# Kernel tuning notes

Measured on AMD Instinct MI355X. Metric: run time of the kernel, lower is better.

## Reference

```python
import jax, jax.numpy as jnp
import numpy as np


def _mlp(x, w1, b1, w2, b2):
    # generic 2-layer MLP (stand-in for ConfiguredModule's combine_mlp / embedding_mlp)
    return jax.nn.gelu(x @ w1 + b1) @ w2 + b2


def setup_inputs() -> dict:
    key = jax.random.key(0)
    ks = jax.random.split(key, 8)
    B, N, A = 8, 128, 64          # molecules, atoms, nfeature
    Rr, Ra = 32, 16               # radial / angular geometry shifts
    P = N * (N - 1) // 2          # 8128 atom pairs
    d_pair, H, nembed = 32, 512, 256

    def rnd(k, shp, scale=1.0):
        return jax.random.normal(k, shp, dtype=jnp.float32) * scale

    return {
        "gr": rnd(ks[0], (B, N, Rr, N), 0.1),
        "ga": rnd(ks[1], (B, N, Ra, P), 0.1),
        "afv": rnd(ks[2], (B, N, A)),
        # combine_mlp: 2A -> 2A -> d_pair
        "cw1": rnd(ks[3], (2 * A, 2 * A), 1.0 / np.sqrt(2 * A)),
        "cb1": jnp.zeros((2 * A,), jnp.float32),
        "cw2": rnd(ks[4], (2 * A, d_pair), 1.0 / np.sqrt(2 * A)),
        "cb2": jnp.zeros((d_pair,), jnp.float32),
        # embedding_mlp: Rr*A + Ra*d_pair -> H -> nembed
        "ew1": rnd(ks[5], (Rr * A + Ra * d_pair, H), 1.0 / np.sqrt(Rr * A + Ra * d_pair)),
        "eb1": jnp.zeros((H,), jnp.float32),
        "ew2": rnd(ks[6], (H, nembed), 1.0 / np.sqrt(H)),
        "eb2": jnp.zeros((nembed,), jnp.float32),
    }


def reference(gr, ga, afv, cw1, cb1, cw2, cb2, ew1, eb1, ew2, eb2):
    B, N, A = afv.shape
    # _combine_afv_1: pairwise outer sum/product, upper-triangular (i<j) pairs.
    # Instead of materializing [B, 2A, N, N] and masking, gather pairs directly
    # (row-major i<j order matches torch's triu boolean-mask indexing).
    ii, jj = jnp.triu_indices(N, k=1)           # [P]
    ai = afv[:, ii, :]                           # [B, P, A]
    aj = afv[:, jj, :]                           # [B, P, A]
    afv_pair = jnp.concatenate([ai + aj, ai * aj], axis=-1)  # [B, P, 2A]
    afv_pair = _mlp(afv_pair, cw1, cb1, cw2, cb2)            # [B, P, d_pair]

    # grv = matmul(gr, afv[:, None]) : [B, N, Rr, N] @ [B, 1, N, A] -> [B, N, Rr, A]
    grv = jnp.einsum('bnrm,bma->bnra', gr, afv).reshape(B, N, -1)
    # gav = matmul(ga, afv_pair[:, None]) : [B, N, Ra, P] @ [B, 1, P, d] -> [B, N, Ra, d]
    gav = jnp.einsum('bnap,bpd->bnad', ga, afv_pair).reshape(B, N, -1)

    aef = _mlp(jnp.concatenate([grv, gav], axis=-1), ew1, eb1, ew2, eb2)  # [B, N, nembed]
    return aef, afv
```

## Files before the change

### kernel.cpp

```cpp
#include <hip/hip_runtime.h>
#include <math.h>

#define BB 8
#define NN 128
#define AA 64
#define RR 32
#define RA 16
#define PP 8128
#define DP 32
#define HH 512
#define EE 256
#define XDIM 2560

static constexpr size_t WS_PAIRT = 0;
static constexpr size_t WS_XB    = WS_PAIRT + (size_t)BB*DP*PP/2;
static constexpr size_t WS_EW1B  = WS_XB + (size_t)BB*NN*XDIM/2;
static constexpr size_t WS_CW1T  = WS_EW1B + (size_t)HH*XDIM/2;
static constexpr size_t WS_CW2T  = WS_CW1T + (size_t)128*128/2;
static constexpr size_t WS_EW2B  = WS_CW2T + (size_t)DP*128/2;
static constexpr size_t WS_HB    = WS_EW2B + (size_t)EE*HH/2;

typedef __attribute__((ext_vector_type(8))) short bf16x8;
typedef __attribute__((ext_vector_type(4))) float f32x4;

__device__ __forceinline__ float gelu_f(float x) {
    float u = 0.7978845608028654f * (x + 0.044715f * x * x * x);
    float au = fabsf(u);
    float e = __expf(-2.0f * au);
    float th = (1.0f - e) / (1.0f + e);
    th = copysignf(th, u);
    return 0.5f * x * (1.0f + th);
}

__device__ __forceinline__ unsigned short f2bf(float x) {
    union { float f; unsigned u; } v; v.f = x;
    unsigned r = v.u + 0x7fffu + ((v.u >> 16) & 1u);
    return (unsigned short)(r >> 16);
}

__device__ __forceinline__ bf16x8 pack_bf16x8(float4 a, float4 b) {
    bf16x8 r;
    r[0] = (short)f2bf(a.x); r[1] = (short)f2bf(a.y);
    r[2] = (short)f2bf(a.z); r[3] = (short)f2bf(a.w);
    r[4] = (short)f2bf(b.x); r[5] = (short)f2bf(b.y);
    r[6] = (short)f2bf(b.z); r[7] = (short)f2bf(b.w);
    return r;
}

__global__ __launch_bounds__(256) void prep_k(
    const float* __restrict__ cw1, const float* __restrict__ cw2,
    unsigned short* __restrict__ cw1T, unsigned short* __restrict__ cw2T)
{
    const int bid = blockIdx.x, t = threadIdx.x;
    if (bid < 16) {
        int idx = bid * 256 + t;
        int n = idx >> 5;
        int k0 = (idx & 31) * 4;
        ushort4 o;
        o.x = f2bf(cw1[(size_t)(k0 + 0) * 128 + n]);
        o.y = f2bf(cw1[(size_t)(k0 + 1) * 128 + n]);
        o.z = f2bf(cw1[(size_t)(k0 + 2) * 128 + n]);
        o.w = f2bf(cw1[(size_t)(k0 + 3) * 128 + n]);
        *(ushort4*)(cw1T + (size_t)n * 128 + k0) = o;
    } else {
        int idx = (bid - 16) * 256 + t;
        int d = idx >> 5;
        int k0 = (idx & 31) * 4;
        ushort4 o;
        o.x = f2bf(cw2[(size_t)(k0 + 0) * DP + d]);
        o.y = f2bf(cw2[(size_t)(k0 + 1) * DP + d]);
        o.z = f2bf(cw2[(size_t)(k0 + 2) * DP + d]);
        o.w = f2bf(cw2[(size_t)(k0 + 3) * DP + d]);
        *(ushort4*)(cw2T + (size_t)d * 128 + k0) = o;
    }
}

__global__ __launch_bounds__(256) void stage1_k(
    const float* __restrict__ afv, const unsigned short* __restrict__ cw1T,
    const float* __restrict__ cb1, const unsigned short* __restrict__ cw2T,
    const float* __restrict__ cb2, unsigned short* __restrict__ pairT)
{
    __shared__ unsigned short sm[16384];
    __shared__ int iis[64], jjs[64];
    const int bid = blockIdx.x;
    const int t = threadIdx.x;
    const int w = t >> 6, lane = t & 63;
    const int lm = lane & 15, lg = lane >> 4;

    const int b = bid / 127;
    const int pbase = (bid % 127) * 64;
    unsigned short* X = sm;
    unsigned short* Hs = sm + 8192;

    if (t < 64) {
        int p = pbase + t;
        int i = 0;
        while (i < 126) {
            int nx = i + 1;
            int off = nx * 127 - (nx * (nx - 1)) / 2;
            if (off <= p) i = nx; else break;
        }
        int off = i * 127 - (i * (i - 1)) / 2;
        iis[t] = i;
        jjs[t] = i + 1 + (p - off);
    }
    __syncthreads();
    {
        int pp = t & 63, seg = t >> 6;
        const float* ar = afv + (size_t)(b * NN + iis[pp]) * AA + seg * 16;
        const float* br = afv + (size_t)(b * NN + jjs[pp]) * AA + seg * 16;
        float4 xa = *(const float4*)(ar),     xb2 = *(const float4*)(ar + 4);
        float4 xc = *(const float4*)(ar + 8), xd = *(const float4*)(ar + 12);
        float4 ya = *(const float4*)(br),     yb = *(const float4*)(br + 4);
        float4 yc = *(const float4*)(br + 8), yd = *(const float4*)(br + 12);
        float4 s0 = make_float4(xa.x + ya.x, xa.y + ya.y, xa.z + ya.z, xa.w + ya.w);
        float4 s1 = make_float4(xb2.x + yb.x, xb2.y + yb.y, xb2.z + yb.z, xb2.w + yb.w);
        float4 s2 = make_float4(xc.x + yc.x, xc.y + yc.y, xc.z + yc.z, xc.w + yc.w);
        float4 s3 = make_float4(xd.x + yd.x, xd.y + yd.y, xd.z + yd.z, xd.w + yd.w);
        float4 p0 = make_float4(xa.x * ya.x, xa.y * ya.y, xa.z * ya.z, xa.w * ya.w);
        float4 p1 = make_float4(xb2.x * yb.x, xb2.y * yb.y, xb2.z * yb.z, xb2.w * yb.w);
        float4 p2 = make_float4(xc.x * yc.x, xc.y * yc.y, xc.z * yc.z, xc.w * yc.w);
        float4 p3 = make_float4(xd.x * yd.x, xd.y * yd.y, xd.z * yd.z, xd.w * yd.w);
        int gs = seg * 2, gp = 8 + seg * 2, sw = pp & 7;
        *(bf16x8*)(X + pp * 128 + (((gs + 0) ^ sw) * 8)) = pack_bf16x8(s0, s1);
        *(bf16x8*)(X + pp * 128 + (((gs + 1) ^ sw) * 8)) = pack_bf16x8(s2, s3);
        *(bf16x8*)(X + pp * 128 + (((gp + 0) ^ sw) * 8)) = pack_bf16x8(p0, p1);
        *(bf16x8*)(X + pp * 128 + (((gp + 1) ^ sw) * 8)) = pack_bf16x8(p2, p3);
    }
    __syncthreads();
    const int wn = w * 32;
    f32x4 acc1[4][2];
    #pragma unroll
    for (int i = 0; i < 4; ++i)
        #pragma unroll
        for (int j = 0; j < 2; ++j) acc1[i][j] = 0.f;
    #pragma unroll
    for (int ks = 0; ks < 4; ++ks) {
        int g = ks * 4 + lg;
        bf16x8 a[4];
        #pragma unroll
        for (int mi = 0; mi < 4; ++mi) {
            int row = mi * 16 + lm;
            a[mi] = *(const bf16x8*)(X + row * 128 + ((g ^ (row & 7)) * 8));
        }
        #pragma unroll
        for (int ni = 0; ni < 2; ++ni) {
            bf16x8 bv = *(const bf16x8*)(cw1T + (size_t)(wn + ni * 16 + lm) * 128 +
                                         ks * 32 + lg * 8);
            #pragma unroll
            for (int mi = 0; mi < 4; ++mi)
                acc1[mi][ni] = __builtin_amdgcn_mfma_f32_16x16x32_bf16(
                    a[mi], bv, acc1[mi][ni], 0, 0, 0);
        }
    }
    #pragma unroll
    for (int ni = 0; ni < 2; ++ni) {
        int n = wn + ni * 16 + lm;
        float bb = cb1[n];
        int gn = n >> 3, ne = n & 7;
        #pragma unroll
        for (int mi = 0; mi < 4; ++mi)
            #pragma unroll
            for (int r = 0; r < 4; ++r) {
                int row = mi * 16 + lg * 4 + r;
                Hs[row * 128 + ((gn ^ (row & 7)) * 8 + ne)] =
                    f2bf(gelu_f(acc1[mi][ni][r] + bb));
            }
    }
    __syncthreads();
    f32x4 acc2[2];
    acc2[0] = 0.f; acc2[1] = 0.f;
    #pragma unroll
    for (int ks = 0; ks < 4; ++ks) {
        int row = w * 16 + lm;
        int g = ks * 4 + lg;
        bf16x8 a2 = *(const bf16x8*)(Hs + row * 128 + ((g ^ (row & 7)) * 8));
        #pragma unroll
        for (int ni = 0; ni < 2; ++ni) {
            bf16x8 bv = *(const bf16x8*)(cw2T + (size_t)(ni * 16 + lm) * 128 +
                                         ks * 32 + lg * 8);
            acc2[ni] = __builtin_amdgcn_mfma_f32_16x16x32_bf16(a2, bv, acc2[ni], 0, 0, 0);
        }
    }
    {
        unsigned short* T = sm;
        __syncthreads();
        #pragma unroll
        for (int ni = 0; ni < 2; ++ni) {
            int d = ni * 16 + lm;
            float bb = cb2[d];
            #pragma unroll
            for (int r = 0; r < 4; ++r) {
                int p = w * 16 + lg * 4 + r;
                T[d * 64 + p] = f2bf(acc2[ni][r] + bb);
            }
        }
        __syncthreads();
        int d = t >> 3, slot = t & 7;
        bf16x8 v = *(const bf16x8*)(T + d * 64 + slot * 8);
        *(bf16x8*)(pairT + ((size_t)b * DP + d) * PP + pbase + slot * 8) = v;
    }
}

__global__ __launch_bounds__(256) void gav_k(
    const float* __restrict__ ga, const unsigned short* __restrict__ pairT,
    unsigned short* __restrict__ Xb,
    const float* __restrict__ gr, const float* __restrict__ afv,
    const float* __restrict__ ew1, unsigned short* __restrict__ ew1bT,
    const float* __restrict__ ew2, unsigned short* __restrict__ ew2bT,
    float* __restrict__ out2)
{
    __shared__ unsigned short sm[16384];
    const int bid = blockIdx.x;
    const int t = threadIdx.x;
    const int w = t >> 6, lane = t & 63;
    const int lm = lane & 15, lg = lane >> 4;

    if (bid >= 2944) {
        int idx = (bid - 2944) * 256 + t;
        float4 v = *(const float4*)(afv + (size_t)idx * 4);
        *(float4*)(out2 + (size_t)idx * 4) = v;
        return;
    }
    if (bid >= 2816) {
        int q = (bid - 2816) * 256 + t;
        int n = q & 255;
        int k0 = (q >> 8) * 4;
        ushort4 o;
        o.x = f2bf(ew2[(size_t)(k0 + 0) * EE + n]);
        o.y = f2bf(ew2[(size_t)(k0 + 1) * EE + n]);
        o.z = f2bf(ew2[(size_t)(k0 + 2) * EE + n]);
        o.w = f2bf(ew2[(size_t)(k0 + 3) * EE + n]);
        *(ushort4*)(ew2bT + (size_t)n * HH + k0) = o;
        return;
    }
    if (bid >= 1536) {
        int q = (bid - 1536) * 256 + t;
        int n = q & 511;
        int k0 = (q >> 9) * 4;
        ushort4 o;
        o.x = f2bf(ew1[(size_t)(k0 + 0) * HH + n]);
        o.y = f2bf(ew1[(size_t)(k0 + 1) * HH + n]);
        o.z = f2bf(ew1[(size_t)(k0 + 2) * HH + n]);
        o.w = f2bf(ew1[(size_t)(k0 + 3) * HH + n]);
        *(ushort4*)(ew1bT + (size_t)n * XDIM + k0) = o;
        return;
    }

    if (bid >= 1024) {
        const int gb = bid - 1024;
        const int b = gb >> 6;
        const int rbase = (gb & 63) * 64;
        const float* gab = gr + ((size_t)b * 4096 + rbase) * NN;
        unsigned short* As  = sm;
        unsigned short* Bs2 = sm + 8192;
        {
            const int srow2 = t >> 2, q4 = t & 3;
            const float* arow = gab + (size_t)srow2 * NN + q4 * 32;
            #pragma unroll
            for (int j = 0; j < 4; ++j) {
                float4 x0 = *(const float4*)(arow + j * 8);
                float4 x1 = *(const float4*)(arow + j * 8 + 4);
                bf16x8 v = pack_bf16x8(x0, x1);
                int g = 4 * q4 + j;
                *(bf16x8*)(As + srow2 * 128 + ((g ^ (srow2 & 7)) * 8)) = v;
            }
        }
        #pragma unroll
        for (int q = 0; q < 8; ++q) {
            int pos = t + q * 256;
            int m = pos >> 4, f4i = pos & 15;
            float4 v = *(const float4*)(afv + (size_t)(b * NN + m) * AA + f4i * 4);
            int gm = m >> 3, me = m & 7;
            float vv[4] = {v.x, v.y, v.z, v.w};
            #pragma unroll
            for (int i = 0; i < 4; ++i) {
                int a = f4i * 4 + i;
                Bs2[a * 128 + ((gm ^ (a & 7)) * 8 + me)] = f2bf(vv[i]);
            }
        }
        __syncthreads();
        const int wm = w * 16;
        f32x4 acc[4];
        #pragma unroll
        for (int j = 0; j < 4; ++j) acc[j] = 0.f;
        #pragma unroll
        for (int ks = 0; ks < 4; ++ks) {
            int g = ks * 4 + lg;
            int r0 = wm + lm;
            bf16x8 a0 = *(const bf16x8*)(As + r0 * 128 + ((g ^ (r0 & 7)) * 8));
            #pragma unroll
            for (int ni = 0; ni < 4; ++ni) {
                int a = ni * 16 + lm;
                bf16x8 bv = *(const bf16x8*)(Bs2 + a * 128 + ((g ^ (a & 7)) * 8));
                acc[ni] = __builtin_amdgcn_mfma_f32_16x16x32_bf16(a0, bv, acc[ni], 0, 0, 0);
            }
        }
        __syncthreads();
        unsigned short* T = sm;
        #pragma unroll
        for (int ni = 0; ni < 4; ++ni)
            #pragma unroll
            for (int r = 0; r < 4; ++r)
                T[(wm + lg * 4 + r) * 64 + ni * 16 + lm] = f2bf(acc[ni][r]);
        __syncthreads();
        #pragma unroll
        for (int q = 0; q < 2; ++q) {
            int idx = t + q * 256;
            int rr2 = idx >> 3, slot = idx & 7;
            bf16x8 v = *(const bf16x8*)(T + rr2 * 64 + slot * 8);
            int grow = rbase + rr2;
            *(bf16x8*)(Xb + ((size_t)(b * NN) + (grow >> 5)) * XDIM +
                       (grow & 31) * 64 + slot * 8) = v;
        }
        return;
    }

    const int b = bid & 7, rt = bid >> 3;
    const int rbase = rt * 16;
    const int srow = t >> 4, slot = t & 15;
    const int bd = t >> 3, bslot = t & 7;
    const int wc = w * 16;

    f32x4 acc = 0.f;

    const float* gab = ga + (size_t)(b * 2048 + rbase) * PP;
    const unsigned short* pbT = pairT + (size_t)b * DP * PP;

    float4 ra0, ra1;
    bf16x8 rb0, rb1;

#define GAV_LOAD(IT)                                                         \
    {                                                                        \
        int kn = (IT) * 128 + slot * 8;                                      \
        if (kn > PP - 8) kn = PP - 8;           \
        ra0 = *(const float4*)(gab + (size_t)srow * PP + kn);                \
        ra1 = *(const float4*)(gab + (size_t)srow * PP + kn + 4);            \
        int kb = (IT) * 128 + bslot * 8;                                     \
        int kb1 = kb + 64; if (kb1 > PP - 8) kb1 = PP - 8;                   \
        rb0 = *(const bf16x8*)(pbT + (size_t)bd * PP + kb);                  \
        rb1 = *(const bf16x8*)(pbT + (size_t)bd * PP + kb1);                 \
    }

#define GAV_WRITE(BUF)                                                      \
    {                                                                        \
        unsigned short* A_ = sm + (BUF) * 6144;                              \
        unsigned short* B_ = A_ + 2048;                                      \
        int gA = slot ^ (srow & 7);                                          \
        *(bf16x8*)(A_ + srow * 128 + gA * 8) = pack_bf16x8(ra0, ra1);        \
        int gB = bslot ^ (bd & 7);                                           \
        *(bf16x8*)(B_ + bd * 128 + gB * 8) = rb0;                            \
        *(bf16x8*)(B_ + bd * 128 + (gB + 8) * 8) = rb1;                      \
    }

    GAV_LOAD(0);
    GAV_WRITE(0);
    __syncthreads();
    GAV_LOAD(1);

    for (int it = 0; it < 64; ++it) {
        const int cur = it & 1;
        const unsigned short* Ac = sm + cur * 6144;
        const unsigned short* Bc = Ac + 2048;
        if (it + 1 < 64) GAV_WRITE(cur ^ 1);
        if (it + 2 < 64) GAV_LOAD(it + 2);
        if (w < 2) {
            const int nk = (it < 63) ? 4 : 2;
            for (int ks = 0; ks < nk; ++ks) {
                int gg = ks * 4 + lg;
                int rowb = wc + lm;
                bf16x8 a  = *(const bf16x8*)(Ac + lm * 128 + ((gg ^ (lm & 7)) * 8));
                bf16x8 bv = *(const bf16x8*)(Bc + rowb * 128 + ((gg ^ (rowb & 7)) * 8));
                acc = __builtin_amdgcn_mfma_f32_16x16x32_bf16(a, bv, acc, 0, 0, 0);
            }
        }
        __syncthreads();
    }
    if (w < 2) {
        #pragma unroll
        for (int r = 0; r < 4; ++r) {
            int a2 = lg * 4 + r;
            Xb[(size_t)(b * NN + rt) * XDIM + 2048 + a2 * DP + wc + lm] = f2bf(acc[r]);
        }
    }
}

__global__ __launch_bounds__(256) void mlp1_k(
    const unsigned short* __restrict__ Xb,
    const unsigned short* __restrict__ Wt,
    const float* __restrict__ eb1, unsigned short* __restrict__ Hb)
{
    __shared__ unsigned short sm[16384];
    const int bid = blockIdx.x;
    const int xcd = bid & 7, idx = bid >> 3;
    const int rt = (xcd << 2) | (idx & 3);
    const int ct = idx >> 2;
    const int rbase = rt * 32, nbase = ct * 32;
    const int t = threadIdx.x;
    const int w = t >> 6, lane = t & 63;
    const int lm = lane & 15, lg = lane >> 4;
    const int wr = (w & 1) * 16, wc = (w >> 1) * 16;
    const int srow = t >> 3, sg = t & 7;

    f32x4 acc = 0.f;

    const unsigned short* Arow = Xb + (size_t)(rbase + srow) * XDIM;
    const unsigned short* Brow = Wt + (size_t)(nbase + srow) * XDIM;

    bf16x8 rA0, rA1, rB0, rB1;

#define M1_LOAD(IT)  { int kn = (IT) * 128 + sg * 8;                         \
                       rA0 = *(const bf16x8*)(Arow + kn);                    \
                       rA1 = *(const bf16x8*)(Arow + kn + 64);               \
                       rB0 = *(const bf16x8*)(Brow + kn);                    \
                       rB1 = *(const bf16x8*)(Brow + kn + 64); }
#define M1_WRITE(BUF) { unsigned short* A_ = sm + (BUF) * 8192;              \
                        unsigned short* B_ = A_ + 4096;                      \
                        int g0 = sg ^ (srow & 7);                            \
                        *(bf16x8*)(A_ + srow * 128 + g0 * 8) = rA0;          \
                        *(bf16x8*)(A_ + srow * 128 + (g0 + 8) * 8) = rA1;    \
                        *(bf16x8*)(B_ + srow * 128 + g0 * 8) = rB0;          \
                        *(bf16x8*)(B_ + srow * 128 + (g0 + 8) * 8) = rB1; }

    M1_LOAD(0); M1_WRITE(0);
    __syncthreads();
    M1_LOAD(1);

    for (int it = 0; it < 20; ++it) {
        const int cur = it & 1;
        const unsigned short* Ac = sm + cur * 8192;
        const unsigned short* Bc = Ac + 4096;
        if (it + 1 < 20) M1_WRITE(cur ^ 1);
        if (it + 2 < 20) M1_LOAD(it + 2);
        #pragma unroll
        for (int ks = 0; ks < 4; ++ks) {
            int g = ks * 4 + lg;
            int r0 = wr + lm, r1 = wc + lm;
            bf16x8 a  = *(const bf16x8*)(Ac + r0 * 128 + ((g ^ (r0 & 7)) * 8));
            bf16x8 bv = *(const bf16x8*)(Bc + r1 * 128 + ((g ^ (r1 & 7)) * 8));
            acc = __builtin_amdgcn_mfma_f32_16x16x32_bf16(a, bv, acc, 0, 0, 0);
        }
        __syncthreads();
    }
    const int col = nbase + wc + lm;
    const float bb = eb1[col];
    #pragma unroll
    for (int r = 0; r < 4; ++r) {
        int row = rbase + wr + lg * 4 + r;
        Hb[(size_t)row * HH + col] = f2bf(gelu_f(acc[r] + bb));
    }
}

__global__ __launch_bounds__(256) void mlp2_k(
    const unsigned short* __restrict__ Hb,
    const unsigned short* __restrict__ Wt,
    const float* __restrict__ eb2, float* __restrict__ out)
{
    __shared__ unsigned short sm[16384];
    const int bid = blockIdx.x;
    const int xcd = bid & 7, idx = bid >> 3;
    const int rt = (xcd << 2) | (idx & 3);
    const int ct = idx >> 2;
    const int rbase = rt * 32, nbase = ct * 32;
    const int t = threadIdx.x;
    const int w = t >> 6, lane = t & 63;
    const int lm = lane & 15, lg = lane >> 4;
    const int wr = (w & 1) * 16, wc = (w >> 1) * 16;
    const int srow = t >> 3, sg = t & 7;

    f32x4 acc = 0.f;

    const unsigned short* Arow = Hb + (size_t)(rbase + srow) * HH;
    const unsigned short* Brow = Wt + (size_t)(nbase + srow) * HH;

    bf16x8 rA0, rA1, rB0, rB1;

#define M2_LOAD(IT)  { int kn = (IT) * 128 + sg * 8;                         \
                       rA0 = *(const bf16x8*)(Arow + kn);                    \
                       rA1 = *(const bf16x8*)(Arow + kn + 64);               \
                       rB0 = *(const bf16x8*)(Brow + kn);                    \
                       rB1 = *(const bf16x8*)(Brow + kn + 64); }
#define M2_WRITE(BUF) { unsigned short* A_ = sm + (BUF) * 8192;              \
                        unsigned short* B_ = A_ + 4096;                      \
                        int g0 = sg ^ (srow & 7);                            \
                        *(bf16x8*)(A_ + srow * 128 + g0 * 8) = rA0;          \
                        *(bf16x8*)(A_ + srow * 128 + (g0 + 8) * 8) = rA1;    \
                        *(bf16x8*)(B_ + srow * 128 + g0 * 8) = rB0;          \
                        *(bf16x8*)(B_ + srow * 128 + (g0 + 8) * 8) = rB1; }

    M2_LOAD(0); M2_WRITE(0);
    __syncthreads();
    M2_LOAD(1);

    for (int it = 0; it < 4; ++it) {
        const int cur = it & 1;
        const unsigned short* Ac = sm + cur * 8192;
        const unsigned short* Bc = Ac + 4096;
        if (it + 1 < 4) M2_WRITE(cur ^ 1);
        if (it + 2 < 4) M2_LOAD(it + 2);
        #pragma unroll
        for (int ks = 0; ks < 4; ++ks) {
            int g = ks * 4 + lg;
            int r0 = wr + lm, r1 = wc + lm;
            bf16x8 a  = *(const bf16x8*)(Ac + r0 * 128 + ((g ^ (r0 & 7)) * 8));
            bf16x8 bv = *(const bf16x8*)(Bc + r1 * 128 + ((g ^ (r1 & 7)) * 8));
            acc = __builtin_amdgcn_mfma_f32_16x16x32_bf16(a, bv, acc, 0, 0, 0);
        }
        __syncthreads();
    }
    const int col = nbase + wc + lm;
    const float bb = eb2[col];
    #pragma unroll
    for (int r = 0; r < 4; ++r) {
        int row = rbase + wr + lg * 4 + r;
        out[(size_t)row * EE + col] = acc[r] + bb;
    }
}

extern "C" void kernel_launch(void* const* d_in, const int* in_sizes, int n_in,
                              void* d_out, int out_size, void* d_ws, size_t ws_size,
                              hipStream_t stream) {
    const float* gr  = (const float*)d_in[0];
    const float* ga  = (const float*)d_in[1];
    const float* afv = (const float*)d_in[2];
    const float* cw1 = (const float*)d_in[3];
    const float* cb1 = (const float*)d_in[4];
    const float* cw2 = (const float*)d_in[5];
    const float* cb2 = (const float*)d_in[6];
    const float* ew1 = (const float*)d_in[7];
    const float* eb1 = (const float*)d_in[8];
    const float* ew2 = (const float*)d_in[9];
    const float* eb2 = (const float*)d_in[10];
    float* out = (float*)d_out;
    float* ws = (float*)d_ws;

    unsigned short* pairT  = (unsigned short*)(ws + WS_PAIRT);
    unsigned short* Xb     = (unsigned short*)(ws + WS_XB);
    unsigned short* ew1bT  = (unsigned short*)(ws + WS_EW1B);
    unsigned short* cw1T   = (unsigned short*)(ws + WS_CW1T);
    unsigned short* cw2T   = (unsigned short*)(ws + WS_CW2T);
    unsigned short* ew2bT  = (unsigned short*)(ws + WS_EW2B);
    unsigned short* Hb     = (unsigned short*)(ws + WS_HB);

    prep_k<<<dim3(20), dim3(256), 0, stream>>>(cw1, cw2, cw1T, cw2T);
    stage1_k<<<dim3(1016), dim3(256), 0, stream>>>(afv, cw1T, cb1, cw2T, cb2, pairT);
    gav_k<<<dim3(3008), dim3(256), 0, stream>>>(ga, pairT, Xb, gr, afv,
                                                ew1, ew1bT, ew2, ew2bT,
                                                out + (size_t)BB * NN * EE);
    mlp1_k<<<dim3(512), dim3(256), 0, stream>>>(Xb, ew1bT, eb1, Hb);
    mlp2_k<<<dim3(256), dim3(256), 0, stream>>>(Hb, ew2bT, eb2, out);
}
```

Before: 162.3 us.

## Rewrite gav GEMM to load operands directly into registers without LDS staging

The gav part of the fused kernel used to stage ga and pairT tiles through double-buffered shared memory, with only 2 of 4 waves issuing MFMAs over 16 rows per block. Now each wave loads its own 16 ga rows and both 16-column halves of pairT straight from global memory into MFMA operand registers, and a block covers 64 rows. This removes the LDS traffic and barriers and keeps all waves doing math. The block count drops from 1024 to 256, and the other branch offsets move to match. The trade-off is less latency hiding without software pipelining, and each wave rereads pairT from global or L2.

```diff
diff --git a/kernel.cpp b/kernel.cpp
--- a/kernel.cpp
+++ b/kernel.cpp
@@ -216,14 +216,14 @@
     const int w = t >> 6, lane = t & 63;
     const int lm = lane & 15, lg = lane >> 4;
 
-    if (bid >= 2944) {
-        int idx = (bid - 2944) * 256 + t;
+    if (bid >= 2176) {
+        int idx = (bid - 2176) * 256 + t;
         float4 v = *(const float4*)(afv + (size_t)idx * 4);
         *(float4*)(out2 + (size_t)idx * 4) = v;
         return;
     }
-    if (bid >= 2816) {
-        int q = (bid - 2816) * 256 + t;
+    if (bid >= 2048) {
+        int q = (bid - 2048) * 256 + t;
         int n = q & 255;
         int k0 = (q >> 8) * 4;
         ushort4 o;
@@ -234,8 +234,8 @@
         *(ushort4*)(ew2bT + (size_t)n * HH + k0) = o;
         return;
     }
-    if (bid >= 1536) {
-        int q = (bid - 1536) * 256 + t;
+    if (bid >= 768) {
+        int q = (bid - 768) * 256 + t;
         int n = q & 511;
         int k0 = (q >> 9) * 4;
         ushort4 o;
@@ -247,8 +247,8 @@
         return;
     }
 
-    if (bid >= 1024) {
-        const int gb = bid - 1024;
+    if (bid >= 256) {
+        const int gb = bid - 256;
         const int b = gb >> 6;
         const int rbase = (gb & 63) * 64;
         const float* gab = gr + ((size_t)b * 4096 + rbase) * NN;
@@ -317,70 +317,50 @@
     }
 
     const int b = bid & 7, rt = bid >> 3;
-    const int rbase = rt * 16;
-    const int srow = t >> 4, slot = t & 15;
-    const int bd = t >> 3, bslot = t & 7;
-    const int wc = w * 16;
-
-    f32x4 acc = 0.f;
-
-    const float* gab = ga + (size_t)(b * 2048 + rbase) * PP;
-    const unsigned short* pbT = pairT + (size_t)b * DP * PP;
-
-    float4 ra0, ra1;
-    bf16x8 rb0, rb1;
-
-#define GAV_LOAD(IT)                                                         \
-    {                                                                        \
-        int kn = (IT) * 128 + slot * 8;                                      \
-        if (kn > PP - 8) kn = PP - 8;           \
-        ra0 = *(const float4*)(gab + (size_t)srow * PP + kn);                \
-        ra1 = *(const float4*)(gab + (size_t)srow * PP + kn + 4);            \
-        int kb = (IT) * 128 + bslot * 8;                                     \
-        int kb1 = kb + 64; if (kb1 > PP - 8) kb1 = PP - 8;                   \
-        rb0 = *(const bf16x8*)(pbT + (size_t)bd * PP + kb);                  \
-        rb1 = *(const bf16x8*)(pbT + (size_t)bd * PP + kb1);                 \
-    }
-
-#define GAV_WRITE(BUF)                                                      \
-    {                                                                        \
-        unsigned short* A_ = sm + (BUF) * 6144;                              \
-        unsigned short* B_ = A_ + 2048;                                      \
-        int gA = slot ^ (srow & 7);                                          \
-        *(bf16x8*)(A_ + srow * 128 + gA * 8) = pack_bf16x8(ra0, ra1);        \
-        int gB = bslot ^ (bd & 7);                                           \
-        *(bf16x8*)(B_ + bd * 128 + gB * 8) = rb0;                            \
-        *(bf16x8*)(B_ + bd * 128 + (gB + 8) * 8) = rb1;                      \
-    }
-
-    GAV_LOAD(0);
-    GAV_WRITE(0);
-    __syncthreads();
-    GAV_LOAD(1);
-
-    for (int it = 0; it < 64; ++it) {
-        const int cur = it & 1;
-        const unsigned short* Ac = sm + cur * 6144;
-        const unsigned short* Bc = Ac + 2048;
-        if (it + 1 < 64) GAV_WRITE(cur ^ 1);
-        if (it + 2 < 64) GAV_LOAD(it + 2);
-        if (w < 2) {
-            const int nk = (it < 63) ? 4 : 2;
-            for (int ks = 0; ks < nk; ++ks) {
-                int gg = ks * 4 + lg;
-                int rowb = wc + lm;
-                bf16x8 a  = *(const bf16x8*)(Ac + lm * 128 + ((gg ^ (lm & 7)) * 8));
-                bf16x8 bv = *(const bf16x8*)(Bc + rowb * 128 + ((gg ^ (rowb & 7)) * 8));
-                acc = __builtin_amdgcn_mfma_f32_16x16x32_bf16(a, bv, acc, 0, 0, 0);
-            }
-        }
-        __syncthreads();
-    }
-    if (w < 2) {
+    const int rbase = rt * 64;
+    const int row = rbase + w * 16 + lm;
+    const float* arow_g = ga + (size_t)(b * 2048 + row) * PP;
+    const unsigned short* b0row = pairT + (size_t)(b * DP + lm) * PP;
+    const unsigned short* b1row = pairT + (size_t)(b * DP + 16 + lm) * PP;
+
+    f32x4 acc0 = 0.f, acc1 = 0.f;
+
+    for (int it = 0; it < 63; ++it) {
+        const int kb = it * 128;
+        #pragma unroll
+        for (int ks = 0; ks < 4; ++ks) {
+            int k = kb + ks * 32 + lg * 8;
+            float4 a0 = *(const float4*)(arow_g + k);
+            float4 a1 = *(const float4*)(arow_g + k + 4);
+            bf16x8 af = pack_bf16x8(a0, a1);
+            bf16x8 bf0 = *(const bf16x8*)(b0row + k);
+            bf16x8 bf1 = *(const bf16x8*)(b1row + k);
+            acc0 = __builtin_amdgcn_mfma_f32_16x16x32_bf16(af, bf0, acc0, 0, 0, 0);
+            acc1 = __builtin_amdgcn_mfma_f32_16x16x32_bf16(af, bf1, acc1, 0, 0, 0);
+        }
+    }
+    {
+        const int kb = 8064;
+        #pragma unroll
+        for (int ks = 0; ks < 2; ++ks) {
+            int k = kb + ks * 32 + lg * 8;
+            float4 a0 = *(const float4*)(arow_g + k);
+            float4 a1 = *(const float4*)(arow_g + k + 4);
+            bf16x8 af = pack_bf16x8(a0, a1);
+            bf16x8 bf0 = *(const bf16x8*)(b0row + k);
+            bf16x8 bf1 = *(const bf16x8*)(b1row + k);
+            acc0 = __builtin_amdgcn_mfma_f32_16x16x32_bf16(af, bf0, acc0, 0, 0, 0);
+            acc1 = __builtin_amdgcn_mfma_f32_16x16x32_bf16(af, bf1, acc1, 0, 0, 0);
+        }
+    }
+    {
+        const int n = rt * 4 + w;
+        unsigned short* xrow = Xb + (size_t)(b * NN + n) * XDIM + 2048;
         #pragma unroll
         for (int r = 0; r < 4; ++r) {
             int a2 = lg * 4 + r;
-            Xb[(size_t)(b * NN + rt) * XDIM + 2048 + a2 * DP + wc + lm] = f2bf(acc[r]);
+            xrow[a2 * DP + lm]      = f2bf(acc0[r]);
+            xrow[a2 * DP + 16 + lm] = f2bf(acc1[r]);
         }
     }
 }
@@ -544,7 +524,7 @@
 
     prep_k<<<dim3(20), dim3(256), 0, stream>>>(cw1, cw2, cw1T, cw2T);
     stage1_k<<<dim3(1016), dim3(256), 0, stream>>>(afv, cw1T, cb1, cw2T, cb2, pairT);
-    gav_k<<<dim3(3008), dim3(256), 0, stream>>>(ga, pairT, Xb, gr, afv,
+    gav_k<<<dim3(2240), dim3(256), 0, stream>>>(ga, pairT, Xb, gr, afv,
                                                 ew1, ew1bT, ew2, ew2bT,
                                                 out + (size_t)BB * NN * EE);
     mlp1_k<<<dim3(512), dim3(256), 0, stream>>>(Xb, ew1bT, eb1, Hb);
```

Result: slower. 192.9 us (+18.9%).
